# Performance work log

Measured on AMD Instinct MI355X. Metric: run time of the kernel, lower is better.

## Reference

```python
import jax, jax.numpy as jnp
import numpy as np

N_EMBD = 1024
N_HEAD = 16
HEAD_DIM = N_EMBD // N_HEAD


def setup_inputs() -> dict:
    key = jax.random.key(0)
    ks = jax.random.split(key, 5)
    B, T, C = 2, 2048, N_EMBD
    scale = 0.02
    return {
        "x": jax.random.normal(ks[0], (B, T, C), dtype=jnp.float32),
        "w_attn": jax.random.normal(ks[1], (C, 3 * C), dtype=jnp.float32) * scale,
        "b_attn": jax.random.normal(ks[2], (3 * C,), dtype=jnp.float32) * scale,
        "w_proj": jax.random.normal(ks[3], (C, C), dtype=jnp.float32) * scale,
        "b_proj": jax.random.normal(ks[4], (C,), dtype=jnp.float32) * scale,
    }


def reference(x, w_attn, b_attn, w_proj, b_proj):
    B, T, C = x.shape
    H, D = N_HEAD, HEAD_DIM
    qkv = x @ w_attn + b_attn  # [B,T,3C]
    q, k, v = jnp.split(qkv, 3, axis=-1)
    # [B,T,C] -> [B,H,T,D]
    q = q.reshape(B, T, H, D).transpose(0, 2, 1, 3)
    k = k.reshape(B, T, H, D).transpose(0, 2, 1, 3)
    v = v.reshape(B, T, H, D).transpose(0, 2, 1, 3)
    scores = jnp.einsum("bhqd,bhkd->bhqk", q, k) / jnp.sqrt(jnp.float32(D))
    causal = jnp.tril(jnp.ones((T, T), dtype=bool))
    scores = jnp.where(causal, scores, jnp.finfo(scores.dtype).min)
    attn = jax.nn.softmax(scores, axis=-1)
    y = jnp.einsum("bhqk,bhkd->bhqd", attn, v)  # [B,H,T,D]
    y = y.transpose(0, 2, 1, 3).reshape(B, T, C)
    return y @ w_proj + b_proj
```

## Files before the change

### kernel.cpp

```cpp
#include <hip/hip_runtime.h>

typedef unsigned short u16;
typedef u16 u16x4 __attribute__((ext_vector_type(4)));
typedef u16 u16x8 __attribute__((ext_vector_type(8)));
typedef __bf16 bf16x8 __attribute__((ext_vector_type(8)));
typedef float floatx4 __attribute__((ext_vector_type(4)));

#define N_EMBD 1024
#define N_HEAD 16
#define HEAD_DIM 64
#define SEQ 2048
#define BATCH 2
#define M_ROWS (BATCH * SEQ)

typedef __attribute__((address_space(1))) const unsigned char ga_t;
typedef __attribute__((address_space(3))) unsigned char la_t;

#if __has_builtin(__builtin_amdgcn_exp2f)
#define EXP2(x) __builtin_amdgcn_exp2f(x)
#else
#define EXP2(x) exp2f(x)
#endif

__device__ __forceinline__ u16 cvt_bf16(float f) {
  return __builtin_bit_cast(u16, (__bf16)f);
}

__global__ __launch_bounds__(256) void prep(const float* __restrict__ x,
                                            u16* __restrict__ xb,
                                            const float* __restrict__ wa,
                                            const float* __restrict__ wp,
                                            u16* __restrict__ outa,
                                            u16* __restrict__ outp) {
  const int bid = blockIdx.x;
  if (bid < 2048) {
    const long i = ((long)bid * 256 + threadIdx.x) * 8;
    const float4 f0 = *(const float4*)&x[i];
    const float4 f1 = *(const float4*)&x[i + 4];
    u16x8 p;
    p[0] = cvt_bf16(f0.x); p[1] = cvt_bf16(f0.y);
    p[2] = cvt_bf16(f0.z); p[3] = cvt_bf16(f0.w);
    p[4] = cvt_bf16(f1.x); p[5] = cvt_bf16(f1.y);
    p[6] = cvt_bf16(f1.z); p[7] = cvt_bf16(f1.w);
    *(u16x8*)&xb[i] = p;
    return;
  }
  __shared__ u16 tile[32][33];
  const int t = bid - 2048;
  const int gx = t & 127;
  const int gy = t >> 7;
  const int R = N_EMBD;
  const float* in;
  u16* out;
  int C, bx;
  if (gx < 96) {
    in = wa; out = outa; C = 3 * N_EMBD; bx = gx * 32;
  } else {
    in = wp; out = outp; C = N_EMBD; bx = (gx - 96) * 32;
  }
  const int by = gy * 32;
  const int tx = threadIdx.x & 31;
  const int ty = threadIdx.x >> 5;
#pragma unroll
  for (int j = 0; j < 32; j += 8)
    tile[ty + j][tx] = cvt_bf16(in[(long)(by + ty + j) * C + bx + tx]);
  __syncthreads();
#pragma unroll
  for (int j = 0; j < 32; j += 8)
    out[(long)(bx + ty + j) * R + by + tx] = tile[tx][ty + j];
}

#define GBK 64

__device__ __forceinline__ void stage192(const u16* __restrict__ A,
                                         const u16* __restrict__ Bt, int bm,
                                         int bn, int kt, int tid, u16* as,
                                         u16* bs) {
#pragma unroll
  for (int i = 0; i < 2; ++i) {
    const int p = tid + 512 * i;
    const int row = p >> 3;
    const int sl = (p & 7) ^ (row & 7);
    const int wb = (i * 512 + (tid & 448)) * 8;
    __builtin_amdgcn_global_load_lds(
        (ga_t*)&A[(long)(bm + row) * N_EMBD + kt + sl * 8], (la_t*)&as[wb], 16,
        0, 0);
  }
#pragma unroll
  for (int i = 0; i < 3; ++i) {
    const int p = tid + 512 * i;
    const int row = p >> 3;
    const int sl = (p & 7) ^ (row & 7);
    const int wb = (i * 512 + (tid & 448)) * 8;
    __builtin_amdgcn_global_load_lds(
        (ga_t*)&Bt[(long)(bn + row) * N_EMBD + kt + sl * 8], (la_t*)&bs[wb], 16,
        0, 0);
  }
}

__global__ __launch_bounds__(512, 4) void gemm_qkv(
    const u16* __restrict__ A, const u16* __restrict__ Bt,
    const float* __restrict__ bias, u16* __restrict__ qo, u16* __restrict__ ko,
    u16* __restrict__ vo) {
  extern __shared__ u16 smem[];
  u16* As = smem;
  u16* Bs = smem + 2 * 128 * 64;
  const int tid = threadIdx.x;

  const int nx = gridDim.x;
  const int nwg = nx * gridDim.y;
  int lin = blockIdx.y * nx + blockIdx.x;
  lin = (lin & 7) * (nwg >> 3) + (lin >> 3);
  const int bm = (lin / nx) * 128;
  const int bn = (lin % nx) * 192;

  const int w = tid >> 6;
  const int l = tid & 63;
  const int wm = (w >> 2) * 64;
  const int wn = (w & 3) * 48;
  const int m16 = l & 15;
  const int quad = l >> 4;
  const int rsw = m16 & 7;

  floatx4 acc[4][3];
#pragma unroll
  for (int i = 0; i < 4; ++i)
#pragma unroll
    for (int j = 0; j < 3; ++j) acc[i][j] = (floatx4){0.f, 0.f, 0.f, 0.f};

  stage192(A, Bt, bm, bn, 0, tid, As, Bs);
  stage192(A, Bt, bm, bn, GBK, tid, As + 128 * 64, Bs + 192 * 64);
  asm volatile("s_waitcnt vmcnt(5)" ::: "memory");
  __builtin_amdgcn_s_barrier();

  for (int kt = 0; kt < 16; ++kt) {
    u16* as = As + (kt & 1) * (128 * 64);
    u16* bs = Bs + (kt & 1) * (192 * 64);

    bf16x8 af[4][2], bf[3][2];
#pragma unroll
    for (int i = 0; i < 4; ++i)
#pragma unroll
      for (int kk = 0; kk < 2; ++kk)
        af[i][kk] = __builtin_bit_cast(
            bf16x8, *(const u16x8*)&as[(wm + i * 16 + m16) * 64 +
                                       (((kk * 4 + quad) ^ rsw) * 8)]);
#pragma unroll
    for (int j = 0; j < 3; ++j)
#pragma unroll
      for (int kk = 0; kk < 2; ++kk)
        bf[j][kk] = __builtin_bit_cast(
            bf16x8, *(const u16x8*)&bs[(wn + j * 16 + m16) * 64 +
                                       (((kk * 4 + quad) ^ rsw) * 8)]);
    asm volatile("s_waitcnt lgkmcnt(0)" ::: "memory");
    __builtin_amdgcn_s_barrier();

    if (kt + 2 < 16) {
      stage192(A, Bt, bm, bn, (kt + 2) * GBK, tid, as, bs);
      asm volatile("s_waitcnt vmcnt(5)" ::: "memory");
    } else {
      asm volatile("s_waitcnt vmcnt(0)" ::: "memory");
    }
    __builtin_amdgcn_s_barrier();

    __builtin_amdgcn_s_setprio(1);
#pragma unroll
    for (int kk = 0; kk < 2; ++kk)
#pragma unroll
      for (int i = 0; i < 4; ++i)
#pragma unroll
        for (int j = 0; j < 3; ++j)
          acc[i][j] = __builtin_amdgcn_mfma_f32_16x16x32_bf16(
              af[i][kk], bf[j][kk], acc[i][j], 0, 0, 0);
    __builtin_amdgcn_s_setprio(0);
  }

#pragma unroll
  for (int i = 0; i < 4; ++i) {
#pragma unroll
    for (int j = 0; j < 3; ++j) {
      const int col = bn + wn + j * 16 + m16;
      const float bv = bias[col];
      const int which = col >> 10;
      const int cc = col & 1023;
      const int h = cc >> 6;
      const int dd = cc & 63;
      const int row0 = bm + wm + i * 16 + quad * 4;
      const int b = row0 >> 11;
      const int t0 = row0 & 2047;
      if (which == 2) {
        u16x4 pk;
#pragma unroll
        for (int r = 0; r < 4; ++r) pk[r] = cvt_bf16(acc[i][j][r] + bv);
        *(u16x4*)&vo[(((long)(b * N_HEAD + h)) * HEAD_DIM + dd) * SEQ + t0] =
            pk;
      } else {
        u16* dst = (which == 0) ? qo : ko;
#pragma unroll
        for (int r = 0; r < 4; ++r)
          dst[(((long)(b * N_HEAD + h)) * SEQ + t0 + r) * HEAD_DIM + dd] =
              cvt_bf16(acc[i][j][r] + bv);
      }
    }
  }
}

#define BK 32

template <int MODE>
__device__ __forceinline__ void stage128(const u16* __restrict__ A,
                                         const u16* __restrict__ Bt, int bm,
                                         int bn, int kt, int K, int tid,
                                         u16* as, u16* bs) {
  const int w = tid >> 6;
  const int l = tid & 63;
  const int lrow = l >> 2;
#pragma unroll
  for (int p = 0; p < 2; ++p) {
    const int arow = p * 64 + w * 16;
    const int row = arow + lrow;
    const int sl = (l & 3) ^ ((row >> 1) & 3);
    long gA;
    if (MODE == 0) {
      gA = (long)(bm + row) * K + kt + sl * 8;
    } else {
      const int m = bm + row;
      const int b = m >> 11, t = m & 2047;
      const int k0 = kt + sl * 8;
      const int head = k0 >> 6, dd = k0 & 63;
      gA = (((long)(b * N_HEAD + head)) * SEQ + t) * HEAD_DIM + dd;
    }
    __builtin_amdgcn_global_load_lds((ga_t*)(A + gA), (la_t*)&as[arow * BK],
                                     16, 0, 0);
  }
  constexpr int TN = (MODE == 1) ? 64 : 128;
#pragma unroll
  for (int p = 0; p < TN / 64; ++p) {
    const int arow = p * 64 + w * 16;
    const int row = arow + lrow;
    const int sl = (l & 3) ^ ((row >> 1) & 3);
    const long gB = (long)(bn + row) * K + kt + sl * 8;
    __builtin_amdgcn_global_load_lds((ga_t*)(Bt + gB), (la_t*)&bs[arow * BK],
                                     16, 0, 0);
  }
}

template <int MODE>
__global__ __launch_bounds__(256) void gemm128(
    const u16* __restrict__ A, const u16* __restrict__ Bt,
    const float* __restrict__ bias, float* __restrict__ out,
    u16* __restrict__ qo, u16* __restrict__ ko, u16* __restrict__ vo, int N,
    int K) {
  constexpr int TN = (MODE == 1) ? 64 : 128;
  constexpr int NJ = TN / 32;
  __shared__ u16 As[3][128 * BK];
  __shared__ u16 Bs[3][TN * BK];
  const int tid = threadIdx.x;

  const int nx = gridDim.x;
  const int nwg = nx * gridDim.y;
  int lin = blockIdx.y * nx + blockIdx.x;
  lin = (lin & 7) * (nwg >> 3) + (lin >> 3);
  const int bm = (lin / nx) * 128;
  const int bn = (lin % nx) * TN;

  const int w = tid >> 6;
  const int l = tid & 63;
  const int wm = (w >> 1) * 64;
  const int wn = (w & 1) * (TN / 2);
  const int m16 = l & 15;
  const int quad = l >> 4;
  const int ksw = (quad ^ ((m16 >> 1) & 3)) * 8;

  floatx4 acc[4][NJ];
#pragma unroll
  for (int i = 0; i < 4; ++i)
#pragma unroll
    for (int j = 0; j < NJ; ++j) acc[i][j] = (floatx4){0.f, 0.f, 0.f, 0.f};

  const int nk = K / BK;
  stage128<MODE>(A, Bt, bm, bn, 0, K, tid, As[0], Bs[0]);
  stage128<MODE>(A, Bt, bm, bn, BK, K, tid, As[1], Bs[1]);

  u16 *a0 = As[0], *a1 = As[1], *a2 = As[2];
  u16 *b0 = Bs[0], *b1 = Bs[1], *b2 = Bs[2];

  for (int t = 0; t < nk; ++t) {
    if (t + 1 < nk) {
      if constexpr (MODE == 0)
        asm volatile("s_waitcnt vmcnt(4)" ::: "memory");
      else
        asm volatile("s_waitcnt vmcnt(3)" ::: "memory");
    } else {
      asm volatile("s_waitcnt vmcnt(0)" ::: "memory");
    }
    __builtin_amdgcn_s_barrier();

    if (t + 2 < nk)
      stage128<MODE>(A, Bt, bm, bn, (t + 2) * BK, K, tid, a2, b2);

    bf16x8 af[4], bfr[NJ];
#pragma unroll
    for (int i = 0; i < 4; ++i)
      af[i] = __builtin_bit_cast(
          bf16x8, *(const u16x8*)&a0[(wm + i * 16 + m16) * BK + ksw]);
#pragma unroll
    for (int j = 0; j < NJ; ++j)
      bfr[j] = __builtin_bit_cast(
          bf16x8, *(const u16x8*)&b0[(wn + j * 16 + m16) * BK + ksw]);
#pragma unroll
    for (int i = 0; i < 4; ++i)
#pragma unroll
      for (int j = 0; j < NJ; ++j)
        acc[i][j] = __builtin_amdgcn_mfma_f32_16x16x32_bf16(af[i], bfr[j],
                                                            acc[i][j], 0, 0, 0);
    u16* ta = a0; a0 = a1; a1 = a2; a2 = ta;
    u16* tb = b0; b0 = b1; b1 = b2; b2 = tb;
  }

#pragma unroll
  for (int i = 0; i < 4; ++i) {
#pragma unroll
    for (int j = 0; j < NJ; ++j) {
      const int col = bn + wn + j * 16 + m16;
      const float bv = bias[col];
      if (MODE == 1) {
#pragma unroll
        for (int r = 0; r < 4; ++r) {
          const int row = bm + wm + i * 16 + quad * 4 + r;
          out[(long)row * N_EMBD + col] = acc[i][j][r] + bv;
        }
      } else {
        const int which = col >> 10;
        const int cc = col & 1023;
        const int h = cc >> 6;
        const int dd = cc & 63;
        const int row0 = bm + wm + i * 16 + quad * 4;
        const int b = row0 >> 11;
        const int t0 = row0 & 2047;
        if (which == 2) {
          u16x4 pk;
#pragma unroll
          for (int r = 0; r < 4; ++r) pk[r] = cvt_bf16(acc[i][j][r] + bv);
          *(u16x4*)&vo[(((long)(b * N_HEAD + h)) * HEAD_DIM + dd) * SEQ + t0] =
              pk;
        } else {
          u16* dst = (which == 0) ? qo : ko;
#pragma unroll
          for (int r = 0; r < 4; ++r)
            dst[(((long)(b * N_HEAD + h)) * SEQ + t0 + r) * HEAD_DIM + dd] =
                cvt_bf16(acc[i][j][r] + bv);
        }
      }
    }
  }
}

#define BQ 64
#define BKV 64
#define LOG2E 1.44269504f
#define NQT (SEQ / BQ)
#define NROWS (32 * SEQ)

__device__ __forceinline__ void stage_kv(const u16* __restrict__ K,
                                         const u16* __restrict__ Vt, long bh,
                                         int kt, int tid, u16* kl, u16* vl) {
#pragma unroll
  for (int i = 0; i < 2; ++i) {
    const int p = tid + 256 * i;
    const int row = p >> 3;
    const int slot = (p & 7) ^ (row & 7);
    const int wb = (i * 256 + (tid & 192)) * 8;
    __builtin_amdgcn_global_load_lds(
        (ga_t*)&K[(bh * SEQ + kt + row) * HEAD_DIM + slot * 8], (la_t*)&kl[wb],
        16, 0, 0);
    __builtin_amdgcn_global_load_lds(
        (ga_t*)&Vt[(bh * HEAD_DIM + row) * SEQ + kt + slot * 8], (la_t*)&vl[wb],
        16, 0, 0);
  }
}

__global__ __launch_bounds__(256, 4) void flash_attn(
    const u16* __restrict__ Qy, const u16* __restrict__ K,
    const u16* __restrict__ Vt, float* __restrict__ Opart,
    float2* __restrict__ mlpart) {
  const int id = blockIdx.x;
  const int a = id >> 6;
  const int h = (id >> 5) & 1;
  const long bh = id & 31;
  const int tid = threadIdx.x;
  const int w = tid >> 6;
  const int l = tid & 63;
  const int m16 = l & 15;
  const int quad = l >> 4;

  __shared__ u16 Kl[2][BKV * 64];
  __shared__ u16 Vl[2][64 * BKV];
  __shared__ u16 Pl[4][16 * 64];

  const float SC = 0.125f * LOG2E;
  const int sw = (m16 & 7) << 3;

  for (int ph = 0; ph < 2; ++ph) {
    const int iq = ph ? (31 - a) : a;
    const int na = iq + 1;
    const int mid = (na + 1) >> 1;
    const int s0 = h ? mid : 0;
    const int e0 = h ? na : mid;
    const int qglob = iq * BQ + w * 16 + m16;

    bf16x8 qf[2];
    {
      const u16* qrow = Qy + (bh * SEQ + qglob) * HEAD_DIM;
      qf[0] = __builtin_bit_cast(bf16x8, *(const u16x8*)&qrow[quad * 8]);
      qf[1] = __builtin_bit_cast(bf16x8, *(const u16x8*)&qrow[32 + quad * 8]);
    }

    floatx4 Oacc[4];
#pragma unroll
    for (int t = 0; t < 4; ++t) Oacc[t] = (floatx4){0.f, 0.f, 0.f, 0.f};
    float mrow = -1e30f, lsum = 0.f;

    if (s0 < e0) {
      stage_kv(K, Vt, bh, s0 * BKV, tid, Kl[0], Vl[0]);
      __syncthreads();

      for (int it = s0; it < e0; ++it) {
        const int buf = (it - s0) & 1;
        const int kt = it * BKV;
        if (it + 1 < e0)
          stage_kv(K, Vt, bh, kt + BKV, tid, Kl[buf ^ 1], Vl[buf ^ 1]);

        floatx4 s[4];
#pragma unroll
        for (int j = 0; j < 4; ++j) s[j] = (floatx4){0.f, 0.f, 0.f, 0.f};
        __builtin_amdgcn_s_setprio(1);
#pragma unroll
        for (int j = 0; j < 4; ++j)
#pragma unroll
          for (int kk = 0; kk < 2; ++kk) {
            const bf16x8 kf = __builtin_bit_cast(
                bf16x8, *(const u16x8*)&Kl[buf][(j * 16 + m16) * 64 +
                                                ((kk * 32 + quad * 8) ^ sw)]);
            s[j] = __builtin_amdgcn_mfma_f32_16x16x32_bf16(kf, qf[kk], s[j], 0,
                                                           0, 0);
          }
        __builtin_amdgcn_s_setprio(0);
        if (it == na - 1) {
#pragma unroll
          for (int j = 0; j < 4; ++j) {
            const int key0 = kt + j * 16 + quad * 4;
#pragma unroll
            for (int r = 0; r < 4; ++r)
              if (key0 + r > qglob) s[j][r] = -1e30f;
          }
        }

        float tm = s[0][0];
#pragma unroll
        for (int j = 0; j < 4; ++j)
#pragma unroll
          for (int r = 0; r < 4; ++r)
            if (j + r) tm = fmaxf(tm, s[j][r]);
        tm = fmaxf(tm, __shfl_xor(tm, 16, 64));
        tm = fmaxf(tm, __shfl_xor(tm, 32, 64));
        const float pm = tm * SC;
        if (!__all(pm <= mrow + 4.f)) {
          const float mn = fmaxf(mrow, pm);
          const float al = EXP2(mrow - mn);
          mrow = mn;
          lsum *= al;
#pragma unroll
          for (int t = 0; t < 4; ++t)
#pragma unroll
            for (int r = 0; r < 4; ++r) Oacc[t][r] *= al;
        }

        float ls = 0.f;
#pragma unroll
        for (int j = 0; j < 4; ++j) {
          u16x4 pk;
#pragma unroll
          for (int r = 0; r < 4; ++r) {
            const float p = EXP2(__builtin_fmaf(s[j][r], SC, -mrow));
            ls += p;
            pk[r] = cvt_bf16(p);
          }
          *(u16x4*)&Pl[w][m16 * 64 + ((j * 16 + quad * 4) ^ sw)] = pk;
        }
        lsum += ls;

        bf16x8 pf[2];
        pf[0] = __builtin_bit_cast(
            bf16x8, *(const u16x8*)&Pl[w][m16 * 64 + ((quad * 8) ^ sw)]);
        pf[1] = __builtin_bit_cast(
            bf16x8, *(const u16x8*)&Pl[w][m16 * 64 + ((32 + quad * 8) ^ sw)]);
        __builtin_amdgcn_s_setprio(1);
#pragma unroll
        for (int t = 0; t < 4; ++t)
#pragma unroll
          for (int kk = 0; kk < 2; ++kk) {
            const bf16x8 vf = __builtin_bit_cast(
                bf16x8, *(const u16x8*)&Vl[buf][(t * 16 + m16) * 64 +
                                                ((kk * 32 + quad * 8) ^ sw)]);
            Oacc[t] = __builtin_amdgcn_mfma_f32_16x16x32_bf16(vf, pf[kk],
                                                              Oacc[t], 0, 0, 0);
          }
        __builtin_amdgcn_s_setprio(0);
        __syncthreads();
      }
    }

    float lt = lsum;
    lt += __shfl_xor(lt, 16, 64);
    lt += __shfl_xor(lt, 32, 64);
    const long row = bh * SEQ + qglob;
    float* Op = Opart + (long)h * NROWS * HEAD_DIM;
#pragma unroll
    for (int t = 0; t < 4; ++t)
      *(floatx4*)&Op[row * HEAD_DIM + t * 16 + quad * 4] = Oacc[t];
    if (quad == 0) mlpart[h * NROWS + row] = make_float2(mrow, lt);
  }
}

__global__ __launch_bounds__(256) void merge_attn(
    const float* __restrict__ Opart, const float2* __restrict__ mlpart,
    u16* __restrict__ Qy) {
  const int bid = blockIdx.x;
  const int bh = (bid & 7) | (((bid >> 10) & 3) << 3);
  const int chunk = (bid >> 3) & 127;
  const int r = threadIdx.x >> 4;
  const int d0 = (threadIdx.x & 15) * 4;
  const long row = (long)bh * SEQ + chunk * 16 + r;
  const float2 A = mlpart[row];
  const float2 B = mlpart[NROWS + row];
  const float M = fmaxf(A.x, B.x);
  const float w0 = EXP2(A.x - M), w1 = EXP2(B.x - M);
  const float inv = 1.f / (w0 * A.y + w1 * B.y);
  const floatx4 o0 = *(const floatx4*)&Opart[row * HEAD_DIM + d0];
  const floatx4 o1 =
      *(const floatx4*)&Opart[(long)NROWS * HEAD_DIM + row * HEAD_DIM + d0];
  u16x4 pk;
#pragma unroll
  for (int i = 0; i < 4; ++i)
    pk[i] = cvt_bf16((w0 * o0[i] + w1 * o1[i]) * inv);
  *(u16x4*)&Qy[row * HEAD_DIM + d0] = pk;
}

extern "C" void kernel_launch(void* const* d_in, const int* in_sizes, int n_in,
                              void* d_out, int out_size, void* d_ws,
                              size_t ws_size, hipStream_t stream) {
  const float* x = (const float*)d_in[0];
  const float* w_attn = (const float*)d_in[1];
  const float* b_attn = (const float*)d_in[2];
  const float* w_proj = (const float*)d_in[3];
  const float* b_proj = (const float*)d_in[4];
  float* out = (float*)d_out;

  char* ws = (char*)d_ws;
  const size_t SZ = (size_t)BATCH * N_HEAD * SEQ * HEAD_DIM * sizeof(u16);
  u16* q = (u16*)(ws);
  u16* k = (u16*)(ws + SZ);
  u16* vT = (u16*)(ws + 2 * SZ);
  u16* wT_a = (u16*)(ws + 3 * SZ);
  u16* wT_p = (u16*)(ws + 3 * SZ + (size_t)3 * N_EMBD * N_EMBD * sizeof(u16));
  u16* xb = (u16*)(ws + 3 * SZ + (size_t)4 * N_EMBD * N_EMBD * sizeof(u16));
  float* Opart = (float*)(ws + (size_t)48 * 1024 * 1024);
  float2* mlpart =
      (float2*)(ws + (size_t)48 * 1024 * 1024 +
                (size_t)2 * NROWS * HEAD_DIM * sizeof(float));

  prep<<<2048 + 4096, 256, 0, stream>>>(x, xb, w_attn, w_proj, wT_a, wT_p);

  gemm_qkv<<<dim3(3 * N_EMBD / 192, M_ROWS / 128), 512,
             (2 * 128 * 64 + 2 * 192 * 64) * sizeof(u16), stream>>>(
      xb, wT_a, b_attn, q, k, vT);

  flash_attn<<<1024, 256, 0, stream>>>(q, k, vT, Opart, mlpart);

  merge_attn<<<4096, 256, 0, stream>>>(Opart, mlpart, q);

  gemm128<1><<<dim3(N_EMBD / 64, M_ROWS / 128), 256, 0, stream>>>(
      q, wT_p, b_proj, out, nullptr, nullptr, nullptr, N_EMBD, N_EMBD);
}
```

Before: 173.7 us.

## Drop split-KV attention and merge kernel; rewrite projection GEMM with BK=64

```diff
diff --git a/kernel.cpp b/kernel.cpp
--- a/kernel.cpp
+++ b/kernel.cpp
@@ -205,56 +205,43 @@
   }
 }
 
-#define BK 32
-
-template <int MODE>
-__device__ __forceinline__ void stage128(const u16* __restrict__ A,
-                                         const u16* __restrict__ Bt, int bm,
-                                         int bn, int kt, int K, int tid,
-                                         u16* as, u16* bs) {
-  const int w = tid >> 6;
-  const int l = tid & 63;
-  const int lrow = l >> 2;
-#pragma unroll
-  for (int p = 0; p < 2; ++p) {
-    const int arow = p * 64 + w * 16;
-    const int row = arow + lrow;
-    const int sl = (l & 3) ^ ((row >> 1) & 3);
-    long gA;
-    if (MODE == 0) {
-      gA = (long)(bm + row) * K + kt + sl * 8;
-    } else {
-      const int m = bm + row;
-      const int b = m >> 11, t = m & 2047;
-      const int k0 = kt + sl * 8;
-      const int head = k0 >> 6, dd = k0 & 63;
-      gA = (((long)(b * N_HEAD + head)) * SEQ + t) * HEAD_DIM + dd;
-    }
-    __builtin_amdgcn_global_load_lds((ga_t*)(A + gA), (la_t*)&as[arow * BK],
-                                     16, 0, 0);
-  }
-  constexpr int TN = (MODE == 1) ? 64 : 128;
-#pragma unroll
-  for (int p = 0; p < TN / 64; ++p) {
-    const int arow = p * 64 + w * 16;
-    const int row = arow + lrow;
-    const int sl = (l & 3) ^ ((row >> 1) & 3);
-    const long gB = (long)(bn + row) * K + kt + sl * 8;
-    __builtin_amdgcn_global_load_lds((ga_t*)(Bt + gB), (la_t*)&bs[arow * BK],
-                                     16, 0, 0);
-  }
-}
-
-template <int MODE>
-__global__ __launch_bounds__(256) void gemm128(
-    const u16* __restrict__ A, const u16* __restrict__ Bt,
-    const float* __restrict__ bias, float* __restrict__ out,
-    u16* __restrict__ qo, u16* __restrict__ ko, u16* __restrict__ vo, int N,
-    int K) {
-  constexpr int TN = (MODE == 1) ? 64 : 128;
-  constexpr int NJ = TN / 32;
-  __shared__ u16 As[3][128 * BK];
-  __shared__ u16 Bs[3][TN * BK];
+#define PBK 64
+
+__device__ __forceinline__ void stage_proj(const u16* __restrict__ A,
+                                           const u16* __restrict__ Bt, int bm,
+                                           int bn, int kt, int tid, u16* as,
+                                           u16* bs) {
+  const int head = kt >> 6;
+#pragma unroll
+  for (int i = 0; i < 4; ++i) {
+    const int p = tid + 256 * i;
+    const int row = p >> 3;
+    const int sl = (p & 7) ^ (row & 7);
+    const int wb = (i * 256 + (tid & 192)) * 8;
+    const int m = bm + row;
+    const int b = m >> 11, t = m & 2047;
+    __builtin_amdgcn_global_load_lds(
+        (ga_t*)&A[(((long)(b * N_HEAD + head)) * SEQ + t) * HEAD_DIM + sl * 8],
+        (la_t*)&as[wb], 16, 0, 0);
+  }
+#pragma unroll
+  for (int i = 0; i < 2; ++i) {
+    const int p = tid + 256 * i;
+    const int row = p >> 3;
+    const int sl = (p & 7) ^ (row & 7);
+    const int wb = (i * 256 + (tid & 192)) * 8;
+    __builtin_amdgcn_global_load_lds(
+        (ga_t*)&Bt[(long)(bn + row) * N_EMBD + kt + sl * 8], (la_t*)&bs[wb], 16,
+        0, 0);
+  }
+}
+
+__global__ __launch_bounds__(256) void gemm_proj(const u16* __restrict__ A,
+                                                 const u16* __restrict__ Bt,
+                                                 const float* __restrict__ bias,
+                                                 float* __restrict__ out) {
+  __shared__ u16 As[2][128 * 64];
+  __shared__ u16 Bs[2][64 * 64];
   const int tid = threadIdx.x;
 
   const int nx = gridDim.x;
@@ -262,95 +249,79 @@
   int lin = blockIdx.y * nx + blockIdx.x;
   lin = (lin & 7) * (nwg >> 3) + (lin >> 3);
   const int bm = (lin / nx) * 128;
-  const int bn = (lin % nx) * TN;
+  const int bn = (lin % nx) * 64;
 
   const int w = tid >> 6;
   const int l = tid & 63;
   const int wm = (w >> 1) * 64;
-  const int wn = (w & 1) * (TN / 2);
+  const int wn = (w & 1) * 32;
   const int m16 = l & 15;
   const int quad = l >> 4;
-  const int ksw = (quad ^ ((m16 >> 1) & 3)) * 8;
-
-  floatx4 acc[4][NJ];
+  const int rsw = m16 & 7;
+
+  floatx4 acc[4][2];
 #pragma unroll
   for (int i = 0; i < 4; ++i)
 #pragma unroll
-    for (int j = 0; j < NJ; ++j) acc[i][j] = (floatx4){0.f, 0.f, 0.f, 0.f};
-
-  const int nk = K / BK;
-  stage128<MODE>(A, Bt, bm, bn, 0, K, tid, As[0], Bs[0]);
-  stage128<MODE>(A, Bt, bm, bn, BK, K, tid, As[1], Bs[1]);
-
-  u16 *a0 = As[0], *a1 = As[1], *a2 = As[2];
-  u16 *b0 = Bs[0], *b1 = Bs[1], *b2 = Bs[2];
-
-  for (int t = 0; t < nk; ++t) {
-    if (t + 1 < nk) {
-      if constexpr (MODE == 0)
-        asm volatile("s_waitcnt vmcnt(4)" ::: "memory");
-      else
-        asm volatile("s_waitcnt vmcnt(3)" ::: "memory");
+    for (int j = 0; j < 2; ++j) acc[i][j] = (floatx4){0.f, 0.f, 0.f, 0.f};
+
+  stage_proj(A, Bt, bm, bn, 0, tid, As[0], Bs[0]);
+  stage_proj(A, Bt, bm, bn, PBK, tid, As[1], Bs[1]);
+  asm volatile("s_waitcnt vmcnt(6)" ::: "memory");
+  __builtin_amdgcn_s_barrier();
+
+  for (int kt = 0; kt < 16; ++kt) {
+    u16* as = As[kt & 1];
+    u16* bs = Bs[kt & 1];
+
+    bf16x8 af[4][2], bf[2][2];
+#pragma unroll
+    for (int i = 0; i < 4; ++i)
+#pragma unroll
+      for (int kk = 0; kk < 2; ++kk)
+        af[i][kk] = __builtin_bit_cast(
+            bf16x8, *(const u16x8*)&as[(wm + i * 16 + m16) * 64 +
+                                       (((kk * 4 + quad) ^ rsw) * 8)]);
+#pragma unroll
+    for (int j = 0; j < 2; ++j)
+#pragma unroll
+      for (int kk = 0; kk < 2; ++kk)
+        bf[j][kk] = __builtin_bit_cast(
+            bf16x8, *(const u16x8*)&bs[(wn + j * 16 + m16) * 64 +
+                                       (((kk * 4 + quad) ^ rsw) * 8)]);
+    asm volatile("s_waitcnt lgkmcnt(0)" ::: "memory");
+    __builtin_amdgcn_s_barrier();
+
+    if (kt + 2 < 16) {
+      stage_proj(A, Bt, bm, bn, (kt + 2) * PBK, tid, as, bs);
+      asm volatile("s_waitcnt vmcnt(6)" ::: "memory");
     } else {
       asm volatile("s_waitcnt vmcnt(0)" ::: "memory");
     }
     __builtin_amdgcn_s_barrier();
 
-    if (t + 2 < nk)
-      stage128<MODE>(A, Bt, bm, bn, (t + 2) * BK, K, tid, a2, b2);
-
-    bf16x8 af[4], bfr[NJ];
-#pragma unroll
-    for (int i = 0; i < 4; ++i)
-      af[i] = __builtin_bit_cast(
-          bf16x8, *(const u16x8*)&a0[(wm + i * 16 + m16) * BK + ksw]);
-#pragma unroll
-    for (int j = 0; j < NJ; ++j)
-      bfr[j] = __builtin_bit_cast(
-          bf16x8, *(const u16x8*)&b0[(wn + j * 16 + m16) * BK + ksw]);
-#pragma unroll
-    for (int i = 0; i < 4; ++i)
-#pragma unroll
-      for (int j = 0; j < NJ; ++j)
-        acc[i][j] = __builtin_amdgcn_mfma_f32_16x16x32_bf16(af[i], bfr[j],
-                                                            acc[i][j], 0, 0, 0);
-    u16* ta = a0; a0 = a1; a1 = a2; a2 = ta;
-    u16* tb = b0; b0 = b1; b1 = b2; b2 = tb;
+    __builtin_amdgcn_s_setprio(1);
+#pragma unroll
+    for (int kk = 0; kk < 2; ++kk)
+#pragma unroll
+      for (int i = 0; i < 4; ++i)
+#pragma unroll
+        for (int j = 0; j < 2; ++j)
+          acc[i][j] = __builtin_amdgcn_mfma_f32_16x16x32_bf16(
+              af[i][kk], bf[j][kk], acc[i][j], 0, 0, 0);
+    __builtin_amdgcn_s_setprio(0);
   }
 
 #pragma unroll
   for (int i = 0; i < 4; ++i) {
 #pragma unroll
-    for (int j = 0; j < NJ; ++j) {
+    for (int j = 0; j < 2; ++j) {
       const int col = bn + wn + j * 16 + m16;
       const float bv = bias[col];
-      if (MODE == 1) {
-#pragma unroll
-        for (int r = 0; r < 4; ++r) {
-          const int row = bm + wm + i * 16 + quad * 4 + r;
-          out[(long)row * N_EMBD + col] = acc[i][j][r] + bv;
-        }
-      } else {
-        const int which = col >> 10;
-        const int cc = col & 1023;
-        const int h = cc >> 6;
-        const int dd = cc & 63;
-        const int row0 = bm + wm + i * 16 + quad * 4;
-        const int b = row0 >> 11;
-        const int t0 = row0 & 2047;
-        if (which == 2) {
-          u16x4 pk;
-#pragma unroll
-          for (int r = 0; r < 4; ++r) pk[r] = cvt_bf16(acc[i][j][r] + bv);
-          *(u16x4*)&vo[(((long)(b * N_HEAD + h)) * HEAD_DIM + dd) * SEQ + t0] =
-              pk;
-        } else {
-          u16* dst = (which == 0) ? qo : ko;
-#pragma unroll
-          for (int r = 0; r < 4; ++r)
-            dst[(((long)(b * N_HEAD + h)) * SEQ + t0 + r) * HEAD_DIM + dd] =
-                cvt_bf16(acc[i][j][r] + bv);
-        }
+#pragma unroll
+      for (int r = 0; r < 4; ++r) {
+        const int row = bm + wm + i * 16 + quad * 4 + r;
+        out[(long)row * N_EMBD + col] = acc[i][j][r] + bv;
       }
     }
   }
@@ -360,7 +331,6 @@
 #define BKV 64
 #define LOG2E 1.44269504f
 #define NQT (SEQ / BQ)
-#define NROWS (32 * SEQ)
 
 __device__ __forceinline__ void stage_kv(const u16* __restrict__ K,
                                          const u16* __restrict__ Vt, long bh,
@@ -381,13 +351,17 @@
 }
 
 __global__ __launch_bounds__(256, 4) void flash_attn(
-    const u16* __restrict__ Qy, const u16* __restrict__ K,
-    const u16* __restrict__ Vt, float* __restrict__ Opart,
-    float2* __restrict__ mlpart) {
+    u16* __restrict__ Qy, const u16* __restrict__ K,
+    const u16* __restrict__ Vt) {
   const int id = blockIdx.x;
-  const int a = id >> 6;
-  const int h = (id >> 5) & 1;
-  const long bh = id & 31;
+  const int r = id >> 8;
+  const int c = id & 255;
+  const int g = c >> 5;
+  const long bh = c & 31;
+  const int iq = (r == 0) ? (31 - g)
+               : (r == 1) ? (16 + g)
+               : (r == 2) ? (15 - g)
+                          : g;
   const int tid = threadIdx.x;
   const int w = tid >> 6;
   const int l = tid & 63;
@@ -399,152 +373,122 @@
   __shared__ u16 Pl[4][16 * 64];
 
   const float SC = 0.125f * LOG2E;
+  const int qb = iq * BQ;
+  const int ntiles = iq + 1;
+  const int qglob = qb + w * 16 + m16;
   const int sw = (m16 & 7) << 3;
 
-  for (int ph = 0; ph < 2; ++ph) {
-    const int iq = ph ? (31 - a) : a;
-    const int na = iq + 1;
-    const int mid = (na + 1) >> 1;
-    const int s0 = h ? mid : 0;
-    const int e0 = h ? na : mid;
-    const int qglob = iq * BQ + w * 16 + m16;
-
-    bf16x8 qf[2];
-    {
-      const u16* qrow = Qy + (bh * SEQ + qglob) * HEAD_DIM;
-      qf[0] = __builtin_bit_cast(bf16x8, *(const u16x8*)&qrow[quad * 8]);
-      qf[1] = __builtin_bit_cast(bf16x8, *(const u16x8*)&qrow[32 + quad * 8]);
-    }
-
-    floatx4 Oacc[4];
-#pragma unroll
-    for (int t = 0; t < 4; ++t) Oacc[t] = (floatx4){0.f, 0.f, 0.f, 0.f};
-    float mrow = -1e30f, lsum = 0.f;
-
-    if (s0 < e0) {
-      stage_kv(K, Vt, bh, s0 * BKV, tid, Kl[0], Vl[0]);
-      __syncthreads();
-
-      for (int it = s0; it < e0; ++it) {
-        const int buf = (it - s0) & 1;
-        const int kt = it * BKV;
-        if (it + 1 < e0)
-          stage_kv(K, Vt, bh, kt + BKV, tid, Kl[buf ^ 1], Vl[buf ^ 1]);
-
-        floatx4 s[4];
-#pragma unroll
-        for (int j = 0; j < 4; ++j) s[j] = (floatx4){0.f, 0.f, 0.f, 0.f};
-        __builtin_amdgcn_s_setprio(1);
-#pragma unroll
-        for (int j = 0; j < 4; ++j)
-#pragma unroll
-          for (int kk = 0; kk < 2; ++kk) {
-            const bf16x8 kf = __builtin_bit_cast(
-                bf16x8, *(const u16x8*)&Kl[buf][(j * 16 + m16) * 64 +
-                                                ((kk * 32 + quad * 8) ^ sw)]);
-            s[j] = __builtin_amdgcn_mfma_f32_16x16x32_bf16(kf, qf[kk], s[j], 0,
-                                                           0, 0);
-          }
-        __builtin_amdgcn_s_setprio(0);
-        if (it == na - 1) {
-#pragma unroll
-          for (int j = 0; j < 4; ++j) {
-            const int key0 = kt + j * 16 + quad * 4;
-#pragma unroll
-            for (int r = 0; r < 4; ++r)
-              if (key0 + r > qglob) s[j][r] = -1e30f;
-          }
-        }
-
-        float tm = s[0][0];
-#pragma unroll
-        for (int j = 0; j < 4; ++j)
-#pragma unroll
-          for (int r = 0; r < 4; ++r)
-            if (j + r) tm = fmaxf(tm, s[j][r]);
-        tm = fmaxf(tm, __shfl_xor(tm, 16, 64));
-        tm = fmaxf(tm, __shfl_xor(tm, 32, 64));
-        const float pm = tm * SC;
-        if (!__all(pm <= mrow + 4.f)) {
-          const float mn = fmaxf(mrow, pm);
-          const float al = EXP2(mrow - mn);
-          mrow = mn;
-          lsum *= al;
-#pragma unroll
-          for (int t = 0; t < 4; ++t)
-#pragma unroll
-            for (int r = 0; r < 4; ++r) Oacc[t][r] *= al;
-        }
-
-        float ls = 0.f;
-#pragma unroll
-        for (int j = 0; j < 4; ++j) {
-          u16x4 pk;
-#pragma unroll
-          for (int r = 0; r < 4; ++r) {
-            const float p = EXP2(__builtin_fmaf(s[j][r], SC, -mrow));
-            ls += p;
-            pk[r] = cvt_bf16(p);
-          }
-          *(u16x4*)&Pl[w][m16 * 64 + ((j * 16 + quad * 4) ^ sw)] = pk;
-        }
-        lsum += ls;
-
-        bf16x8 pf[2];
-        pf[0] = __builtin_bit_cast(
-            bf16x8, *(const u16x8*)&Pl[w][m16 * 64 + ((quad * 8) ^ sw)]);
-        pf[1] = __builtin_bit_cast(
-            bf16x8, *(const u16x8*)&Pl[w][m16 * 64 + ((32 + quad * 8) ^ sw)]);
-        __builtin_amdgcn_s_setprio(1);
-#pragma unroll
-        for (int t = 0; t < 4; ++t)
-#pragma unroll
-          for (int kk = 0; kk < 2; ++kk) {
-            const bf16x8 vf = __builtin_bit_cast(
-                bf16x8, *(const u16x8*)&Vl[buf][(t * 16 + m16) * 64 +
-                                                ((kk * 32 + quad * 8) ^ sw)]);
-            Oacc[t] = __builtin_amdgcn_mfma_f32_16x16x32_bf16(vf, pf[kk],
-                                                              Oacc[t], 0, 0, 0);
-          }
-        __builtin_amdgcn_s_setprio(0);
-        __syncthreads();
+  bf16x8 qf[2];
+  {
+    const u16* qrow = Qy + (bh * SEQ + qglob) * HEAD_DIM;
+    qf[0] = __builtin_bit_cast(bf16x8, *(const u16x8*)&qrow[quad * 8]);
+    qf[1] = __builtin_bit_cast(bf16x8, *(const u16x8*)&qrow[32 + quad * 8]);
+  }
+
+  floatx4 Oacc[4];
+#pragma unroll
+  for (int t = 0; t < 4; ++t) Oacc[t] = (floatx4){0.f, 0.f, 0.f, 0.f};
+  float mrow = -1e30f, lsum = 0.f;
+
+  stage_kv(K, Vt, bh, 0, tid, Kl[0], Vl[0]);
+  __syncthreads();
+
+  for (int it = 0; it < ntiles; ++it) {
+    const int buf = it & 1;
+    const int kt = it * BKV;
+    if (it + 1 < ntiles)
+      stage_kv(K, Vt, bh, kt + BKV, tid, Kl[buf ^ 1], Vl[buf ^ 1]);
+
+    floatx4 s[4];
+#pragma unroll
+    for (int j = 0; j < 4; ++j) s[j] = (floatx4){0.f, 0.f, 0.f, 0.f};
+    __builtin_amdgcn_s_setprio(1);
+#pragma unroll
+    for (int j = 0; j < 4; ++j)
+#pragma unroll
+      for (int kk = 0; kk < 2; ++kk) {
+        const bf16x8 kf = __builtin_bit_cast(
+            bf16x8, *(const u16x8*)&Kl[buf][(j * 16 + m16) * 64 +
+                                            ((kk * 32 + quad * 8) ^ sw)]);
+        s[j] = __builtin_amdgcn_mfma_f32_16x16x32_bf16(kf, qf[kk], s[j], 0, 0,
+                                                       0);
       }
-    }
-
-    float lt = lsum;
-    lt += __shfl_xor(lt, 16, 64);
-    lt += __shfl_xor(lt, 32, 64);
-    const long row = bh * SEQ + qglob;
-    float* Op = Opart + (long)h * NROWS * HEAD_DIM;
+    __builtin_amdgcn_s_setprio(0);
+    if (it == ntiles - 1) {
+#pragma unroll
+      for (int j = 0; j < 4; ++j) {
+        const int key0 = kt + j * 16 + quad * 4;
+#pragma unroll
+        for (int r = 0; r < 4; ++r)
+          if (key0 + r > qglob) s[j][r] = -1e30f;
+      }
+    }
+
+    float tm = s[0][0];
+#pragma unroll
+    for (int j = 0; j < 4; ++j)
+#pragma unroll
+      for (int r = 0; r < 4; ++r)
+        if (j + r) tm = fmaxf(tm, s[j][r]);
+    tm = fmaxf(tm, __shfl_xor(tm, 16, 64));
+    tm = fmaxf(tm, __shfl_xor(tm, 32, 64));
+    const float pm = tm * SC;
+    if (!__all(pm <= mrow + 4.f)) {
+      const float mn = fmaxf(mrow, pm);
+      const float al = EXP2(mrow - mn);
+      mrow = mn;
+      lsum *= al;
+#pragma unroll
+      for (int t = 0; t < 4; ++t)
+#pragma unroll
+        for (int r = 0; r < 4; ++r) Oacc[t][r] *= al;
+    }
+
+    float ls = 0.f;
+#pragma unroll
+    for (int j = 0; j < 4; ++j) {
+      u16x4 pk;
+#pragma unroll
+      for (int r = 0; r < 4; ++r) {
+        const float p = EXP2(__builtin_fmaf(s[j][r], SC, -mrow));
+        ls += p;
+        pk[r] = cvt_bf16(p);
+      }
+      *(u16x4*)&Pl[w][m16 * 64 + ((j * 16 + quad * 4) ^ sw)] = pk;
+    }
+    lsum += ls;
+
+    bf16x8 pf[2];
+    pf[0] = __builtin_bit_cast(
+        bf16x8, *(const u16x8*)&Pl[w][m16 * 64 + ((quad * 8) ^ sw)]);
+    pf[1] = __builtin_bit_cast(
+        bf16x8, *(const u16x8*)&Pl[w][m16 * 64 + ((32 + quad * 8) ^ sw)]);
+    __builtin_amdgcn_s_setprio(1);
 #pragma unroll
     for (int t = 0; t < 4; ++t)
-      *(floatx4*)&Op[row * HEAD_DIM + t * 16 + quad * 4] = Oacc[t];
-    if (quad == 0) mlpart[h * NROWS + row] = make_float2(mrow, lt);
-  }
-}
-
-__global__ __launch_bounds__(256) void merge_attn(
-    const float* __restrict__ Opart, const float2* __restrict__ mlpart,
-    u16* __restrict__ Qy) {
-  const int bid = blockIdx.x;
-  const int bh = (bid & 7) | (((bid >> 10) & 3) << 3);
-  const int chunk = (bid >> 3) & 127;
-  const int r = threadIdx.x >> 4;
-  const int d0 = (threadIdx.x & 15) * 4;
-  const long row = (long)bh * SEQ + chunk * 16 + r;
-  const float2 A = mlpart[row];
-  const float2 B = mlpart[NROWS + row];
-  const float M = fmaxf(A.x, B.x);
-  const float w0 = EXP2(A.x - M), w1 = EXP2(B.x - M);
-  const float inv = 1.f / (w0 * A.y + w1 * B.y);
-  const floatx4 o0 = *(const floatx4*)&Opart[row * HEAD_DIM + d0];
-  const floatx4 o1 =
-      *(const floatx4*)&Opart[(long)NROWS * HEAD_DIM + row * HEAD_DIM + d0];
-  u16x4 pk;
-#pragma unroll
-  for (int i = 0; i < 4; ++i)
-    pk[i] = cvt_bf16((w0 * o0[i] + w1 * o1[i]) * inv);
-  *(u16x4*)&Qy[row * HEAD_DIM + d0] = pk;
+#pragma unroll
+      for (int kk = 0; kk < 2; ++kk) {
+        const bf16x8 vf = __builtin_bit_cast(
+            bf16x8, *(const u16x8*)&Vl[buf][(t * 16 + m16) * 64 +
+                                            ((kk * 32 + quad * 8) ^ sw)]);
+        Oacc[t] = __builtin_amdgcn_mfma_f32_16x16x32_bf16(vf, pf[kk], Oacc[t],
+                                                          0, 0, 0);
+      }
+    __builtin_amdgcn_s_setprio(0);
+    __syncthreads();
+  }
+
+  float lt = lsum;
+  lt += __shfl_xor(lt, 16, 64);
+  lt += __shfl_xor(lt, 32, 64);
+  const float invl = 1.f / lt;
+#pragma unroll
+  for (int t = 0; t < 4; ++t) {
+    u16x4 pk;
+#pragma unroll
+    for (int r = 0; r < 4; ++r) pk[r] = cvt_bf16(Oacc[t][r] * invl);
+    *(u16x4*)&Qy[(bh * SEQ + qglob) * HEAD_DIM + t * 16 + quad * 4] = pk;
+  }
 }
 
 extern "C" void kernel_launch(void* const* d_in, const int* in_sizes, int n_in,
@@ -565,10 +509,6 @@
   u16* wT_a = (u16*)(ws + 3 * SZ);
   u16* wT_p = (u16*)(ws + 3 * SZ + (size_t)3 * N_EMBD * N_EMBD * sizeof(u16));
   u16* xb = (u16*)(ws + 3 * SZ + (size_t)4 * N_EMBD * N_EMBD * sizeof(u16));
-  float* Opart = (float*)(ws + (size_t)48 * 1024 * 1024);
-  float2* mlpart =
-      (float2*)(ws + (size_t)48 * 1024 * 1024 +
-                (size_t)2 * NROWS * HEAD_DIM * sizeof(float));
 
   prep<<<2048 + 4096, 256, 0, stream>>>(x, xb, w_attn, w_proj, wT_a, wT_p);
 
@@ -576,10 +516,8 @@
              (2 * 128 * 64 + 2 * 192 * 64) * sizeof(u16), stream>>>(
       xb, wT_a, b_attn, q, k, vT);
 
-  flash_attn<<<1024, 256, 0, stream>>>(q, k, vT, Opart, mlpart);
-
-  merge_attn<<<4096, 256, 0, stream>>>(Opart, mlpart, q);
-
-  gemm128<1><<<dim3(N_EMBD / 64, M_ROWS / 128), 256, 0, stream>>>(
-      q, wT_p, b_proj, out, nullptr, nullptr, nullptr, N_EMBD, N_EMBD);
-}
+  flash_attn<<<NQT * 32, 256, 0, stream>>>(q, k, vT);
+
+  gemm_proj<<<dim3(N_EMBD / 64, M_ROWS / 128), 256, 0, stream>>>(
+      q, wT_p, b_proj, out);
+}
```

Measured after the change: 171.0 us. No clear change (-1.5%).
